# Performance work log

Measured on AMD Instinct MI355X. Metric: run time of the kernel, lower is better.

Reference implementation:

```python
import jax, jax.numpy as jnp
import numpy as np

RADIUS2 = 1.0   # radius=1 -> radius^2
NSAMPLE = 4
EPS = 1e-5


def _ball_group(new_xyz, xyz, feats):
    """Per-batch radius ball query + feature grouping.
    new_xyz: (Nq,3), xyz: (Ns,3), feats: (Ns,C) -> (Nq, NSAMPLE, C)."""
    Ns = xyz.shape[0]
    # squared distances via gemm form to avoid a (Nq,Ns,3) intermediate
    d2 = (jnp.sum(new_xyz**2, -1)[:, None] + jnp.sum(xyz**2, -1)[None, :]
          - 2.0 * new_xyz @ xyz.T)                      # (Nq, Ns)
    within = d2 < RADIUS2
    # first NSAMPLE in-radius indices, in point order (pcdet semantics)
    scores = jnp.where(within, -jnp.arange(Ns, dtype=jnp.int32), -Ns)
    vals, _ = jax.lax.top_k(scores, NSAMPLE)
    idx = -vals                                         # (Nq, NSAMPLE); Ns == invalid slot
    valid = idx < Ns
    empty = ~valid[:, 0]                                # no neighbor at all
    idx = jnp.where(valid, idx, idx[:, :1])             # pad with first found neighbor
    idx = jnp.where(empty[:, None], 0, idx)
    grouped = feats[idx]                                # (Nq, NSAMPLE, C) irregular gather
    return jnp.where(empty[:, None, None], 0.0, grouped)


def _bn(x, g, b, axes):
    # BatchNorm1d training-mode stats (biased var); channel axis = 1
    m = jnp.mean(x, axes, keepdims=True)
    v = jnp.var(x, axes, keepdims=True)
    shape = [1] * x.ndim
    shape[1] = -1
    return g.reshape(shape) * (x - m) * jax.lax.rsqrt(v + EPS) + b.reshape(shape)


def _forward(x, conv1_w, conv1_b, bn_g, bn_b, fc1_w, fc1_b, fc_ce_w, fc_ce_b,
             fc2_w, fc2_b, fc_lwh_w, fc_lwh_b, fc3_w, fc3_b, fc_theta_w, fc_theta_b):
    B, T, N, C = x.shape
    new_xyz = x[:, 0, :, :3]                              # (B, N, 3) query points
    xyz = x[:, 1:, :, :3].reshape(B, (T - 1) * N, 3)      # (B, Ns, 3) source points
    feats = x[:, 1:].reshape(B, (T - 1) * N, C)           # (B, Ns, C) source features
    grouped = jax.vmap(_ball_group)(new_xyz, xyz, feats)  # (B, N, NSAMPLE, C)
    g = grouped.reshape(B * N, NSAMPLE, C).transpose(0, 2, 1)  # (M, C, NSAMPLE)
    # shared conv1d (kernel=1) + BN + max-pool over the group
    h = jnp.einsum('mcs,oc->mos', g, conv1_w) + conv1_b[None, :, None]
    h = _bn(h, bn_g, bn_b, (0, 2))
    h = jnp.max(h, axis=-1)                               # (M, D)
    feature = h.reshape(B, N, -1)
    # three FC heads, all reusing bn1 (as in the original module)
    x1 = jax.nn.relu(_bn(h @ fc1_w.T + fc1_b, bn_g, bn_b, (0,)))
    x_ce = x1 @ fc_ce_w.T + fc_ce_b
    x2 = jax.nn.relu(_bn(h @ fc2_w.T + fc2_b, bn_g, bn_b, (0,)))
    x_lwh = x2 @ fc_lwh_w.T + fc_lwh_b
    x3 = jax.nn.relu(_bn(h @ fc3_w.T + fc3_b, bn_g, bn_b, (0,)))
    x_th = x3 @ fc_theta_w.T + fc_theta_b
    out = jnp.concatenate([x_ce, x_lwh, x_th], -1).reshape(B, N, 7)
    return out, feature


def setup_inputs() -> dict:
    key = jax.random.key(0)
    ks = jax.random.split(key, 16)
    B, T, N, C, D = 2, 5, 4096, 16, 128
    x = jax.random.normal(ks[0], (B, T, N, C), jnp.float32)
    w = lambda k, s: jax.random.normal(k, s, jnp.float32) * 0.05
    return dict(
        x=x,
        conv1_w=w(ks[1], (D, C)), conv1_b=w(ks[2], (D,)),
        bn_g=jnp.ones((D,), jnp.float32), bn_b=jnp.zeros((D,), jnp.float32),
        fc1_w=w(ks[3], (D, D)), fc1_b=w(ks[4], (D,)),
        fc_ce_w=w(ks[5], (3, D)), fc_ce_b=w(ks[6], (3,)),
        fc2_w=w(ks[7], (D, D)), fc2_b=w(ks[8], (D,)),
        fc_lwh_w=w(ks[9], (3, D)), fc_lwh_b=w(ks[10], (3,)),
        fc3_w=w(ks[11], (D, D)), fc3_b=w(ks[12], (D,)),
        fc_theta_w=w(ks[13], (1, D)), fc_theta_b=w(ks[14], (1,)),
    )


def reference(x, conv1_w, conv1_b, bn_g, bn_b, fc1_w, fc1_b, fc_ce_w, fc_ce_b,
              fc2_w, fc2_b, fc_lwh_w, fc_lwh_b, fc3_w, fc3_b, fc_theta_w, fc_theta_b):
    return _forward(x, conv1_w, conv1_b, bn_g, bn_b, fc1_w, fc1_b, fc_ce_w, fc_ce_b,
                    fc2_w, fc2_b, fc_lwh_w, fc_lwh_b, fc3_w, fc3_b, fc_theta_w, fc_theta_b)
```

## Files before the change

### kernel.cpp

```cpp
#include <hip/hip_runtime.h>

#define B_   2
#define T_   5
#define N_   4096
#define C_   16
#define D_   128
#define S_   4
#define NS_  16384
#define M_   8192
#define EPS_ 1e-5f
#define NPART 32

#define HX_OFF   0u
#define HN_OFF   1048576u
#define Y_OFF    2097152u
#define ST_OFF   5242880u
#define WL_OFF   5275648u
#define ID4_OFF  5283848u
#define WP_OFF   5316616u
#define PK_OFF   5365768u

#define OUT_FEAT 57344

__global__ __launch_bounds__(256) void k_prep(const float* __restrict__ x,
                                              const float* __restrict__ fw1,
                                              const float* __restrict__ fw2,
                                              const float* __restrict__ fw3,
                                              float* __restrict__ st,
                                              int* __restrict__ wcnt,
                                              float4* __restrict__ wp,
                                              float4* __restrict__ pk4) {
    int tid = threadIdx.x;
    if (blockIdx.x < 128) {
        int row = blockIdx.x * 256 + tid;
        int b = row >> 14, j = row & 16383;
        const float* p = x + (size_t)b * (T_ * N_ * C_) + N_ * C_ + (size_t)j * 16;
        float4 v = *(const float4*)p;
        float pn = (v.x * v.x + v.y * v.y) + v.z * v.z;
        pk4[row] = make_float4(v.x, v.y, v.z, pn);
        return;
    }
    int pb = blockIdx.x - 128;
    int t0 = pb * 256 + tid;
    #pragma unroll
    for (int i = 0; i < 8; i++) st[t0 + 4096 * i] = 0.0f;
    if (pb == 0 && tid == 0) wcnt[0] = 0;
    int o = t0 >> 5, c4 = t0 & 31;
    const float* fws[3] = { fw1, fw2, fw3 };
    #pragma unroll
    for (int k = 0; k < 3; k++)
        wp[k * 4096 + c4 * 128 + o] = *(const float4*)(fws[k] + o * 128 + c4 * 4);
}

__global__ __launch_bounds__(256) void k_ball1(const float* __restrict__ x,
                                               const float* __restrict__ w,
                                               const float* __restrict__ bias,
                                               const float4* __restrict__ pk4,
                                               float* __restrict__ hx,
                                               float* __restrict__ hn,
                                               float* __restrict__ st,
                                               int* __restrict__ wcnt,
                                               int* __restrict__ wl,
                                               int4* __restrict__ id4) {
    int tid = threadIdx.x;
    int wid = tid >> 6, lane = tid & 63;
    __shared__ float red[2][512];

    float wc0[16], wc1[16];
    #pragma unroll
    for (int j = 0; j < 4; j++) {
        float4 a = *(const float4*)(w + lane * 16 + j * 4);
        float4 b2 = *(const float4*)(w + (lane + 64) * 16 + j * 4);
        wc0[j*4+0] = a.x;  wc0[j*4+1] = a.y;  wc0[j*4+2] = a.z;  wc0[j*4+3] = a.w;
        wc1[j*4+0] = b2.x; wc1[j*4+1] = b2.y; wc1[j*4+2] = b2.z; wc1[j*4+3] = b2.w;
    }
    float bo0 = bias[lane], bo1 = bias[lane + 64];

    float asum0 = 0.0f, asq0 = 0.0f, asum1 = 0.0f, asq1 = 0.0f;
    for (int qi = 0; qi < 4; qi++) {
        int m = (blockIdx.x * 4 + wid) * 4 + qi;
        int b = m >> 12, q = m & (N_ - 1);
        const float* xb = x + (size_t)b * (T_ * N_ * C_);
        const float* pts = xb + N_ * C_;
        const float4* pk = pk4 + b * 16384;
        float qx = xb[q * 16 + 0];
        float qy = xb[q * 16 + 1];
        float qz = xb[q * 16 + 2];
        float qn = (qx * qx + qy * qy) + qz * qz;

        float4 pv[8];
        #pragma unroll
        for (int u = 0; u < 8; u++) pv[u] = pk[u * 64 + lane];
        unsigned long long mk[8];
        #pragma unroll
        for (int u = 0; u < 8; u++) {
            float dot = (qx * pv[u].x + qy * pv[u].y) + qz * pv[u].z;
            mk[u] = __ballot((qn + pv[u].w) - 2.0f * dot < 1.0f);
        }

        int i0 = 0, i1 = 0, i2 = 0, i3 = 0, cnt = 0;
        unsigned long long m0 = mk[0];
        if (__builtin_popcountll(m0) >= 4) {
            i0 = __builtin_ctzll(m0); m0 &= m0 - 1;
            i1 = __builtin_ctzll(m0); m0 &= m0 - 1;
            i2 = __builtin_ctzll(m0); m0 &= m0 - 1;
            i3 = __builtin_ctzll(m0);
            cnt = 4;
        } else {
            #pragma unroll
            for (int u = 0; u < 8; u++) {
                unsigned long long mask = mk[u];
                while (mask && cnt < 4) {
                    int id = u * 64 + __builtin_ctzll(mask);
                    if (cnt == 0)      i0 = id;
                    else if (cnt == 1) i1 = id;
                    else if (cnt == 2) i2 = id;
                    else               i3 = id;
                    cnt++;
                    mask &= (mask - 1);
                }
            }
        }

        if (cnt >= 4) {
            int ids[4] = {i0, i1, i2, i3};
            float a0[4], a1[4];
            #pragma unroll
            for (int s = 0; s < 4; s++) {
                const float* rp = pts + (size_t)ids[s] * 16;
                float4 r0 = *(const float4*)(rp);
                float4 r1 = *(const float4*)(rp + 4);
                float4 r2 = *(const float4*)(rp + 8);
                float4 r3 = *(const float4*)(rp + 12);
                float s0 = bo0, s1 = bo1;
                s0 += wc0[0] * r0.x;  s0 += wc0[1] * r0.y;  s0 += wc0[2] * r0.z;  s0 += wc0[3] * r0.w;
                s0 += wc0[4] * r1.x;  s0 += wc0[5] * r1.y;  s0 += wc0[6] * r1.z;  s0 += wc0[7] * r1.w;
                s0 += wc0[8] * r2.x;  s0 += wc0[9] * r2.y;  s0 += wc0[10] * r2.z; s0 += wc0[11] * r2.w;
                s0 += wc0[12] * r3.x; s0 += wc0[13] * r3.y; s0 += wc0[14] * r3.z; s0 += wc0[15] * r3.w;
                s1 += wc1[0] * r0.x;  s1 += wc1[1] * r0.y;  s1 += wc1[2] * r0.z;  s1 += wc1[3] * r0.w;
                s1 += wc1[4] * r1.x;  s1 += wc1[5] * r1.y;  s1 += wc1[6] * r1.z;  s1 += wc1[7] * r1.w;
                s1 += wc1[8] * r2.x;  s1 += wc1[9] * r2.y;  s1 += wc1[10] * r2.z; s1 += wc1[11] * r2.w;
                s1 += wc1[12] * r3.x; s1 += wc1[13] * r3.y; s1 += wc1[14] * r3.z; s1 += wc1[15] * r3.w;
                a0[s] = s0; a1[s] = s1;
            }
            hx[(size_t)m * 128 + lane]      = fmaxf(fmaxf(a0[0], a0[1]), fmaxf(a0[2], a0[3]));
            hx[(size_t)m * 128 + 64 + lane] = fmaxf(fmaxf(a1[0], a1[1]), fmaxf(a1[2], a1[3]));
            hn[(size_t)m * 128 + lane]      = fminf(fminf(a0[0], a0[1]), fminf(a0[2], a0[3]));
            hn[(size_t)m * 128 + 64 + lane] = fminf(fminf(a1[0], a1[1]), fminf(a1[2], a1[3]));
            asum0 += (a0[0] + a0[1]) + (a0[2] + a0[3]);
            asq0  += (a0[0] * a0[0] + a0[1] * a0[1]) + (a0[2] * a0[2] + a0[3] * a0[3]);
            asum1 += (a1[0] + a1[1]) + (a1[2] + a1[3]);
            asq1  += (a1[0] * a1[0] + a1[1] * a1[1]) + (a1[2] * a1[2] + a1[3] * a1[3]);
        } else {
            if (lane == 0) {
                int idx = atomicAdd(wcnt, 1);
                wl[idx] = m;
                id4[m] = make_int4(i0, i1, i2, cnt);
            }
        }
    }

    red[0][wid * 128 + lane]      = asum0;
    red[0][wid * 128 + 64 + lane] = asum1;
    red[1][wid * 128 + lane]      = asq0;
    red[1][wid * 128 + 64 + lane] = asq1;
    __syncthreads();
    if (tid < 128) {
        float* stp = st + (blockIdx.x & (NPART - 1)) * 256;
        float s0 = (red[0][tid] + red[0][128 + tid]) + (red[0][256 + tid] + red[0][384 + tid]);
        float s1 = (red[1][tid] + red[1][128 + tid]) + (red[1][256 + tid] + red[1][384 + tid]);
        atomicAdd(&stp[tid], s0);
        atomicAdd(&stp[128 + tid], s1);
    }
}

__global__ __launch_bounds__(256) void k_ball2(const float* __restrict__ x,
                                               const float* __restrict__ w,
                                               const float* __restrict__ bias,
                                               const float4* __restrict__ pk4,
                                               float* __restrict__ hx,
                                               float* __restrict__ hn,
                                               float* __restrict__ st,
                                               const int* __restrict__ wcnt,
                                               const int* __restrict__ wl,
                                               const int4* __restrict__ id4) {
    int tid = threadIdx.x;
    int wid = tid >> 6, lane = tid & 63;
    __shared__ int sCnt[4];
    __shared__ int sIds[4][4];

    float wc0[16], wc1[16];
    float bo0 = 0.0f, bo1 = 0.0f;
    if (wid == 0) {
        #pragma unroll
        for (int j = 0; j < 4; j++) {
            float4 a = *(const float4*)(w + lane * 16 + j * 4);
            float4 b2 = *(const float4*)(w + (lane + 64) * 16 + j * 4);
            wc0[j*4+0] = a.x;  wc0[j*4+1] = a.y;  wc0[j*4+2] = a.z;  wc0[j*4+3] = a.w;
            wc1[j*4+0] = b2.x; wc1[j*4+1] = b2.y; wc1[j*4+2] = b2.z; wc1[j*4+3] = b2.w;
        }
        bo0 = bias[lane]; bo1 = bias[lane + 64];
    }
    float asum0 = 0.0f, asq0 = 0.0f, asum1 = 0.0f, asq1 = 0.0f;

    int nstrag = *wcnt;
    for (int e = blockIdx.x; e < nstrag; e += gridDim.x) {
        int m = wl[e];
        int b = m >> 12, q = m & (N_ - 1);
        const float* xb = x + (size_t)b * (T_ * N_ * C_);
        const float* pts = xb + N_ * C_;
        const float4* pk = pk4 + b * 16384;
        float qx = xb[q * 16 + 0];
        float qy = xb[q * 16 + 1];
        float qz = xb[q * 16 + 2];
        float qn = (qx * qx + qy * qy) + qz * qz;

        int cstart = 1 + 8 * wid;
        int cend = cstart + 8; if (cend > 32) cend = 32;
        int y0 = 0, y1 = 0, y2 = 0, y3 = 0;
        int myc = 0;
        for (int c = cstart; c < cend && myc < 4; c += 2) {
            bool two = (c + 1 < cend);
            float4 pva[8], pvb[8];
            #pragma unroll
            for (int u = 0; u < 8; u++) pva[u] = pk[c * 512 + u * 64 + lane];
            if (two) {
                #pragma unroll
                for (int u = 0; u < 8; u++) pvb[u] = pk[(c + 1) * 512 + u * 64 + lane];
            }
            unsigned long long ma[8], mb[8];
            #pragma unroll
            for (int u = 0; u < 8; u++) {
                float dot = (qx * pva[u].x + qy * pva[u].y) + qz * pva[u].z;
                ma[u] = __ballot((qn + pva[u].w) - 2.0f * dot < 1.0f);
            }
            if (two) {
                #pragma unroll
                for (int u = 0; u < 8; u++) {
                    float dot = (qx * pvb[u].x + qy * pvb[u].y) + qz * pvb[u].z;
                    mb[u] = __ballot((qn + pvb[u].w) - 2.0f * dot < 1.0f);
                }
            }
            #pragma unroll
            for (int u = 0; u < 8; u++) {
                unsigned long long mask = ma[u];
                while (mask && myc < 4) {
                    int id = c * 512 + u * 64 + __builtin_ctzll(mask);
                    if (myc == 0)      y0 = id;
                    else if (myc == 1) y1 = id;
                    else if (myc == 2) y2 = id;
                    else               y3 = id;
                    myc++;
                    mask &= (mask - 1);
                }
            }
            if (two) {
                #pragma unroll
                for (int u = 0; u < 8; u++) {
                    unsigned long long mask = mb[u];
                    while (mask && myc < 4) {
                        int id = (c + 1) * 512 + u * 64 + __builtin_ctzll(mask);
                        if (myc == 0)      y0 = id;
                        else if (myc == 1) y1 = id;
                        else if (myc == 2) y2 = id;
                        else               y3 = id;
                        myc++;
                        mask &= (mask - 1);
                    }
                }
            }
        }
        if (lane == 0) {
            sCnt[wid] = myc;
            sIds[wid][0] = y0; sIds[wid][1] = y1;
            sIds[wid][2] = y2; sIds[wid][3] = y3;
        }
        __syncthreads();

        if (wid == 0) {
            int4 p1 = id4[m];
            int f0 = 0, f1 = 0, f2 = 0, f3 = 0;
            int fc = p1.w;
            if (fc > 0) f0 = p1.x;
            if (fc > 1) f1 = p1.y;
            if (fc > 2) f2 = p1.z;
            #pragma unroll
            for (int w2 = 0; w2 < 4; w2++) {
                int c2 = sCnt[w2];
                #pragma unroll
                for (int i = 0; i < 4; i++) {
                    if (i < c2 && fc < 4) {
                        int id = sIds[w2][i];
                        if (fc == 0)      f0 = id;
                        else if (fc == 1) f1 = id;
                        else if (fc == 2) f2 = id;
                        else              f3 = id;
                        fc++;
                    }
                }
            }
            if (fc >= 1) {
                if (fc <= 1) f1 = f0;
                if (fc <= 2) f2 = f0;
                if (fc <= 3) f3 = f0;
            }
            int fin[4] = {f0, f1, f2, f3};
            float a0[4], a1[4];
            if (fc == 0) {
                #pragma unroll
                for (int s = 0; s < 4; s++) { a0[s] = bo0; a1[s] = bo1; }
            } else {
                #pragma unroll
                for (int s = 0; s < 4; s++) {
                    const float* rp = pts + (size_t)fin[s] * 16;
                    float4 r0 = *(const float4*)(rp);
                    float4 r1 = *(const float4*)(rp + 4);
                    float4 r2 = *(const float4*)(rp + 8);
                    float4 r3 = *(const float4*)(rp + 12);
                    float s0 = bo0, s1 = bo1;
                    s0 += wc0[0] * r0.x;  s0 += wc0[1] * r0.y;  s0 += wc0[2] * r0.z;  s0 += wc0[3] * r0.w;
                    s0 += wc0[4] * r1.x;  s0 += wc0[5] * r1.y;  s0 += wc0[6] * r1.z;  s0 += wc0[7] * r1.w;
                    s0 += wc0[8] * r2.x;  s0 += wc0[9] * r2.y;  s0 += wc0[10] * r2.z; s0 += wc0[11] * r2.w;
                    s0 += wc0[12] * r3.x; s0 += wc0[13] * r3.y; s0 += wc0[14] * r3.z; s0 += wc0[15] * r3.w;
                    s1 += wc1[0] * r0.x;  s1 += wc1[1] * r0.y;  s1 += wc1[2] * r0.z;  s1 += wc1[3] * r0.w;
                    s1 += wc1[4] * r1.x;  s1 += wc1[5] * r1.y;  s1 += wc1[6] * r1.z;  s1 += wc1[7] * r1.w;
                    s1 += wc1[8] * r2.x;  s1 += wc1[9] * r2.y;  s1 += wc1[10] * r2.z; s1 += wc1[11] * r2.w;
                    s1 += wc1[12] * r3.x; s1 += wc1[13] * r3.y; s1 += wc1[14] * r3.z; s1 += wc1[15] * r3.w;
                    a0[s] = s0; a1[s] = s1;
                }
            }
            hx[(size_t)m * 128 + lane]      = fmaxf(fmaxf(a0[0], a0[1]), fmaxf(a0[2], a0[3]));
            hx[(size_t)m * 128 + 64 + lane] = fmaxf(fmaxf(a1[0], a1[1]), fmaxf(a1[2], a1[3]));
            hn[(size_t)m * 128 + lane]      = fminf(fminf(a0[0], a0[1]), fminf(a0[2], a0[3]));
            hn[(size_t)m * 128 + 64 + lane] = fminf(fminf(a1[0], a1[1]), fminf(a1[2], a1[3]));
            asum0 += (a0[0] + a0[1]) + (a0[2] + a0[3]);
            asq0  += (a0[0] * a0[0] + a0[1] * a0[1]) + (a0[2] * a0[2] + a0[3] * a0[3]);
            asum1 += (a1[0] + a1[1]) + (a1[2] + a1[3]);
            asq1  += (a1[0] * a1[0] + a1[1] * a1[1]) + (a1[2] * a1[2] + a1[3] * a1[3]);
        }
        __syncthreads();
    }
    if (wid == 0 && (int)blockIdx.x < nstrag) {
        float* stp = st + (blockIdx.x & (NPART - 1)) * 256;
        atomicAdd(&stp[lane], asum0);
        atomicAdd(&stp[64 + lane], asum1);
        atomicAdd(&stp[128 + lane], asq0);
        atomicAdd(&stp[192 + lane], asq1);
    }
}

__global__ __launch_bounds__(256) void k_fc(const float* __restrict__ hx,
                                            const float* __restrict__ hn,
                                            float* __restrict__ st,
                                            const float4* __restrict__ wp,
                                            const float* __restrict__ b1,
                                            const float* __restrict__ b2,
                                            const float* __restrict__ b3,
                                            const float* __restrict__ bng,
                                            const float* __restrict__ bnb,
                                            float* __restrict__ y,
                                            float* __restrict__ out) {
    int tid = threadIdx.x;
    int m0 = blockIdx.x * 16;
    __shared__ float hs[2048];
    __shared__ float scsh[256];

    if (tid < 128) {
        float s = 0.0f, q2 = 0.0f;
        #pragma unroll
        for (int p = 0; p < NPART; p++) {
            s  += st[p * 256 + tid];
            q2 += st[p * 256 + 128 + tid];
        }
        float mean = s * (1.0f / 32768.0f);
        float var = q2 * (1.0f / 32768.0f) - mean * mean;
        float sc = bng[tid] / sqrtf(fmaxf(var, 0.0f) + EPS_);
        scsh[tid] = sc;
        scsh[128 + tid] = bnb[tid] - mean * sc;
    }
    __syncthreads();

    for (int i = tid; i < 16 * 128; i += 256) {
        int ml = i >> 7, o = i & 127;
        float vx = hx[(size_t)(m0 + ml) * 128 + o];
        float vn = hn[(size_t)(m0 + ml) * 128 + o];
        float sc = scsh[o];
        float r = fmaxf(sc * vx, sc * vn) + scsh[128 + o];
        hs[ml * 128 + o] = r;
        out[(size_t)OUT_FEAT + (size_t)(m0 + ml) * 128 + o] = r;
    }
    __syncthreads();

    int o = tid & 127, gr = tid >> 7;
    int mbase = gr * 8;
    float acc[3][8];
    {
        float bb0 = b1[o], bb1 = b2[o], bb2 = b3[o];
        #pragma unroll
        for (int mm = 0; mm < 8; mm++) {
            acc[0][mm] = bb0; acc[1][mm] = bb1; acc[2][mm] = bb2;
        }
    }
    for (int c4 = 0; c4 < 32; c4++) {
        float4 w1v = wp[c4 * 128 + o];
        float4 w2v = wp[4096 + c4 * 128 + o];
        float4 w3v = wp[8192 + c4 * 128 + o];
        const float* hp = &hs[mbase * 128 + c4 * 4];
        #pragma unroll
        for (int mm = 0; mm < 8; mm++) {
            float4 hv = *(const float4*)(hp + mm * 128);
            acc[0][mm] += w1v.x * hv.x; acc[0][mm] += w1v.y * hv.y;
            acc[0][mm] += w1v.z * hv.z; acc[0][mm] += w1v.w * hv.w;
            acc[1][mm] += w2v.x * hv.x; acc[1][mm] += w2v.y * hv.y;
            acc[1][mm] += w2v.z * hv.z; acc[1][mm] += w2v.w * hv.w;
            acc[2][mm] += w3v.x * hv.x; acc[2][mm] += w3v.y * hv.y;
            acc[2][mm] += w3v.z * hv.z; acc[2][mm] += w3v.w * hv.w;
        }
    }
    __syncthreads();
    float psum[3], psq[3];
    #pragma unroll
    for (int k = 0; k < 3; k++) {
        float s = 0.0f, sq = 0.0f;
        float* yk = y + (size_t)k * M_ * 128;
        #pragma unroll
        for (int mm = 0; mm < 8; mm++) {
            float v = acc[k][mm];
            yk[(size_t)(m0 + mbase + mm) * 128 + o] = v;
            s += v; sq += v * v;
        }
        psum[k] = s; psq[k] = sq;
    }
    #pragma unroll
    for (int k = 0; k < 3; k++) {
        hs[(k * 2 + gr) * 128 + o] = psum[k];
        hs[768 + (k * 2 + gr) * 128 + o] = psq[k];
    }
    __syncthreads();
    float* bp = st + 8192 + (blockIdx.x & (NPART - 1)) * 768;
    for (int t = tid; t < 384; t += 256) {
        int k = t >> 7, oo = t & 127;
        float s  = hs[(k * 2) * 128 + oo] + hs[(k * 2 + 1) * 128 + oo];
        float sq = hs[768 + (k * 2) * 128 + oo] + hs[768 + (k * 2 + 1) * 128 + oo];
        atomicAdd(&bp[k * 256 + oo], s);
        atomicAdd(&bp[k * 256 + 128 + oo], sq);
    }
}

__global__ __launch_bounds__(256) void k_heads(const float* __restrict__ y,
                                               const float* __restrict__ st,
                                               const float* __restrict__ wce, const float* __restrict__ bce,
                                               const float* __restrict__ wlwh, const float* __restrict__ blwh,
                                               const float* __restrict__ wth, const float* __restrict__ bth,
                                               const float* __restrict__ bng, const float* __restrict__ bnb,
                                               float* __restrict__ out) {
    int tid = threadIdx.x;
    __shared__ float bsc[768];
    for (int t = tid; t < 384; t += 256) {
        int k = t >> 7, o = t & 127;
        float s = 0.0f, q2 = 0.0f;
        #pragma unroll
        for (int p = 0; p < NPART; p++) {
            const float* bp = st + 8192 + p * 768 + k * 256;
            s  += bp[o];
            q2 += bp[128 + o];
        }
        float mean = s * (1.0f / 8192.0f);
        float var = q2 * (1.0f / 8192.0f) - mean * mean;
        float sc = bng[o] / sqrtf(fmaxf(var, 0.0f) + EPS_);
        bsc[k * 256 + o] = sc;
        bsc[k * 256 + 128 + o] = bnb[o] - mean * sc;
    }
    __syncthreads();

    int wave = tid >> 6, lane = tid & 63;
    const float* y1 = y;
    const float* y2 = y + (size_t)M_ * D_;
    const float* y3 = y + 2 * (size_t)M_ * D_;
    #pragma unroll
    for (int i = 0; i < 4; i++) {
        int m = blockIdx.x * 16 + wave * 4 + i;
        float p[7] = {0, 0, 0, 0, 0, 0, 0};
        #pragma unroll
        for (int cc = 0; cc < 2; cc++) {
            int c = lane + 64 * cc;
            float v1 = fmaxf(y1[(size_t)m * D_ + c] * bsc[c] + bsc[128 + c], 0.0f);
            float v2 = fmaxf(y2[(size_t)m * D_ + c] * bsc[256 + c] + bsc[384 + c], 0.0f);
            float v3 = fmaxf(y3[(size_t)m * D_ + c] * bsc[512 + c] + bsc[640 + c], 0.0f);
            p[0] += v1 * wce[c];
            p[1] += v1 * wce[128 + c];
            p[2] += v1 * wce[256 + c];
            p[3] += v2 * wlwh[c];
            p[4] += v2 * wlwh[128 + c];
            p[5] += v2 * wlwh[256 + c];
            p[6] += v3 * wth[c];
        }
        #pragma unroll
        for (int off = 32; off > 0; off >>= 1) {
            #pragma unroll
            for (int j = 0; j < 7; j++) p[j] += __shfl_xor(p[j], off);
        }
        if (lane == 0) {
            out[m * 7 + 0] = p[0] + bce[0];
            out[m * 7 + 1] = p[1] + bce[1];
            out[m * 7 + 2] = p[2] + bce[2];
            out[m * 7 + 3] = p[3] + blwh[0];
            out[m * 7 + 4] = p[4] + blwh[1];
            out[m * 7 + 5] = p[5] + blwh[2];
            out[m * 7 + 6] = p[6] + bth[0];
        }
    }
}

extern "C" void kernel_launch(void* const* d_in, const int* in_sizes, int n_in,
                              void* d_out, int out_size, void* d_ws, size_t ws_size,
                              hipStream_t stream) {
    (void)in_sizes; (void)n_in; (void)out_size; (void)ws_size;
    const float* x        = (const float*)d_in[0];
    const float* conv1_w  = (const float*)d_in[1];
    const float* conv1_b  = (const float*)d_in[2];
    const float* bn_g     = (const float*)d_in[3];
    const float* bn_b     = (const float*)d_in[4];
    const float* fc1_w    = (const float*)d_in[5];
    const float* fc1_b    = (const float*)d_in[6];
    const float* fc_ce_w  = (const float*)d_in[7];
    const float* fc_ce_b  = (const float*)d_in[8];
    const float* fc2_w    = (const float*)d_in[9];
    const float* fc2_b    = (const float*)d_in[10];
    const float* fc_lwh_w = (const float*)d_in[11];
    const float* fc_lwh_b = (const float*)d_in[12];
    const float* fc3_w    = (const float*)d_in[13];
    const float* fc3_b    = (const float*)d_in[14];
    const float* fc_th_w  = (const float*)d_in[15];
    const float* fc_th_b  = (const float*)d_in[16];

    float* ws = (float*)d_ws;
    float* hx = ws + HX_OFF;
    float* hn = ws + HN_OFF;
    float* y  = ws + Y_OFF;
    float* st = ws + ST_OFF;
    int*  wcnt = (int*)(ws + WL_OFF);
    int*  wl   = wcnt + 1;
    int4* id4  = (int4*)(ws + ID4_OFF);
    float4* wp  = (float4*)(ws + WP_OFF);
    float4* pk4 = (float4*)(ws + PK_OFF);
    float* out = (float*)d_out;

    hipLaunchKernelGGL(k_prep,  dim3(144),  dim3(256), 0, stream,
                       x, fc1_w, fc2_w, fc3_w, st, wcnt, wp, pk4);
    hipLaunchKernelGGL(k_ball1, dim3(512),  dim3(256), 0, stream,
                       x, conv1_w, conv1_b, pk4, hx, hn, st, wcnt, wl, id4);
    hipLaunchKernelGGL(k_ball2, dim3(512),  dim3(256), 0, stream,
                       x, conv1_w, conv1_b, pk4, hx, hn, st, wcnt, wl, id4);
    hipLaunchKernelGGL(k_fc,    dim3(512),  dim3(256), 0, stream, hx, hn, st, wp,
                       fc1_b, fc2_b, fc3_b, bn_g, bn_b, y, out);
    hipLaunchKernelGGL(k_heads, dim3(512),  dim3(256), 0, stream, y, st,
                       fc_ce_w, fc_ce_b, fc_lwh_w, fc_lwh_b, fc_th_w, fc_th_b, bn_g, bn_b, out);
}
```

Before: 146.9 us.

## Fuse all five stages into one cooperative kernel with grid syncs

Folds prep, ball-query passes, FC and heads into a single cooperative kernel of 512 blocks, with grid-wide barriers between phases in place of separate kernel launches. The intent is to remove per-launch overhead and the gaps between dependent kernels. The fused kernel needs all 512 blocks resident at once and is capped at two blocks per SM by its launch bounds, which can raise register pressure; if the cooperative launch fails, the separate kernels run instead. The prep phase was rewritten to fit a 512-block grid using a global thread index.

```diff
diff --git a/kernel.cpp b/kernel.cpp
--- a/kernel.cpp
+++ b/kernel.cpp
@@ -1,4 +1,7 @@
 #include <hip/hip_runtime.h>
+#include <hip/hip_cooperative_groups.h>
+
+namespace cg = cooperative_groups;
 
 #define B_   2
 #define T_   5
@@ -22,49 +25,44 @@
 
 #define OUT_FEAT 57344
 
-__global__ __launch_bounds__(256) void k_prep(const float* __restrict__ x,
-                                              const float* __restrict__ fw1,
-                                              const float* __restrict__ fw2,
-                                              const float* __restrict__ fw3,
-                                              float* __restrict__ st,
-                                              int* __restrict__ wcnt,
-                                              float4* __restrict__ wp,
-                                              float4* __restrict__ pk4) {
-    int tid = threadIdx.x;
-    if (blockIdx.x < 128) {
-        int row = blockIdx.x * 256 + tid;
-        int b = row >> 14, j = row & 16383;
+
+__device__ __forceinline__ void prep_phase(int bid, int tid,
+    const float* __restrict__ x,
+    const float* __restrict__ fw1, const float* __restrict__ fw2,
+    const float* __restrict__ fw3,
+    float* __restrict__ st, int* __restrict__ wcnt,
+    float4* __restrict__ wp, float4* __restrict__ pk4)
+{
+    int gtid = bid * 256 + tid;
+    if (gtid < 32768) {
+        int b = gtid >> 14, j = gtid & 16383;
         const float* p = x + (size_t)b * (T_ * N_ * C_) + N_ * C_ + (size_t)j * 16;
         float4 v = *(const float4*)p;
         float pn = (v.x * v.x + v.y * v.y) + v.z * v.z;
-        pk4[row] = make_float4(v.x, v.y, v.z, pn);
-        return;
-    }
-    int pb = blockIdx.x - 128;
-    int t0 = pb * 256 + tid;
-    #pragma unroll
-    for (int i = 0; i < 8; i++) st[t0 + 4096 * i] = 0.0f;
-    if (pb == 0 && tid == 0) wcnt[0] = 0;
-    int o = t0 >> 5, c4 = t0 & 31;
-    const float* fws[3] = { fw1, fw2, fw3 };
-    #pragma unroll
-    for (int k = 0; k < 3; k++)
-        wp[k * 4096 + c4 * 128 + o] = *(const float4*)(fws[k] + o * 128 + c4 * 4);
-}
-
-__global__ __launch_bounds__(256) void k_ball1(const float* __restrict__ x,
-                                               const float* __restrict__ w,
-                                               const float* __restrict__ bias,
-                                               const float4* __restrict__ pk4,
-                                               float* __restrict__ hx,
-                                               float* __restrict__ hn,
-                                               float* __restrict__ st,
-                                               int* __restrict__ wcnt,
-                                               int* __restrict__ wl,
-                                               int4* __restrict__ id4) {
-    int tid = threadIdx.x;
+        pk4[gtid] = make_float4(v.x, v.y, v.z, pn);
+    }
+    if (gtid < 4096) {
+        #pragma unroll
+        for (int i = 0; i < 8; i++) st[gtid + 4096 * i] = 0.0f;
+    }
+    if (gtid == 0) wcnt[0] = 0;
+    if (gtid < 12288) {
+        int k = gtid >> 12, t0 = gtid & 4095;
+        int o = t0 >> 5, c4 = t0 & 31;
+        const float* fw = (k == 0) ? fw1 : ((k == 1) ? fw2 : fw3);
+        wp[k * 4096 + c4 * 128 + o] = *(const float4*)(fw + o * 128 + c4 * 4);
+    }
+}
+
+__device__ __forceinline__ void ball1_phase(int bid, int tid, float* smem,
+    const float* __restrict__ x, const float* __restrict__ w,
+    const float* __restrict__ bias, const float4* __restrict__ pk4,
+    float* __restrict__ hx, float* __restrict__ hn, float* __restrict__ st,
+    int* __restrict__ wcnt, int* __restrict__ wl, int4* __restrict__ id4)
+{
     int wid = tid >> 6, lane = tid & 63;
-    __shared__ float red[2][512];
+    float* red0 = smem;
+    float* red1 = smem + 512;
 
     float wc0[16], wc1[16];
     #pragma unroll
@@ -78,7 +76,7 @@
 
     float asum0 = 0.0f, asq0 = 0.0f, asum1 = 0.0f, asq1 = 0.0f;
     for (int qi = 0; qi < 4; qi++) {
-        int m = (blockIdx.x * 4 + wid) * 4 + qi;
+        int m = (bid * 4 + wid) * 4 + qi;
         int b = m >> 12, q = m & (N_ - 1);
         const float* xb = x + (size_t)b * (T_ * N_ * C_);
         const float* pts = xb + N_ * C_;
@@ -160,34 +158,30 @@
         }
     }
 
-    red[0][wid * 128 + lane]      = asum0;
-    red[0][wid * 128 + 64 + lane] = asum1;
-    red[1][wid * 128 + lane]      = asq0;
-    red[1][wid * 128 + 64 + lane] = asq1;
+    red0[wid * 128 + lane]      = asum0;
+    red0[wid * 128 + 64 + lane] = asum1;
+    red1[wid * 128 + lane]      = asq0;
+    red1[wid * 128 + 64 + lane] = asq1;
     __syncthreads();
     if (tid < 128) {
-        float* stp = st + (blockIdx.x & (NPART - 1)) * 256;
-        float s0 = (red[0][tid] + red[0][128 + tid]) + (red[0][256 + tid] + red[0][384 + tid]);
-        float s1 = (red[1][tid] + red[1][128 + tid]) + (red[1][256 + tid] + red[1][384 + tid]);
+        float* stp = st + (bid & (NPART - 1)) * 256;
+        float s0 = (red0[tid] + red0[128 + tid]) + (red0[256 + tid] + red0[384 + tid]);
+        float s1 = (red1[tid] + red1[128 + tid]) + (red1[256 + tid] + red1[384 + tid]);
         atomicAdd(&stp[tid], s0);
         atomicAdd(&stp[128 + tid], s1);
     }
 }
 
-__global__ __launch_bounds__(256) void k_ball2(const float* __restrict__ x,
-                                               const float* __restrict__ w,
-                                               const float* __restrict__ bias,
-                                               const float4* __restrict__ pk4,
-                                               float* __restrict__ hx,
-                                               float* __restrict__ hn,
-                                               float* __restrict__ st,
-                                               const int* __restrict__ wcnt,
-                                               const int* __restrict__ wl,
-                                               const int4* __restrict__ id4) {
-    int tid = threadIdx.x;
+__device__ __forceinline__ void ball2_phase(int bid, int tid, float* smem,
+    const float* __restrict__ x, const float* __restrict__ w,
+    const float* __restrict__ bias, const float4* __restrict__ pk4,
+    float* __restrict__ hx, float* __restrict__ hn, float* __restrict__ st,
+    const int* __restrict__ wcnt, const int* __restrict__ wl,
+    const int4* __restrict__ id4)
+{
     int wid = tid >> 6, lane = tid & 63;
-    __shared__ int sCnt[4];
-    __shared__ int sIds[4][4];
+    int* sCnt = (int*)smem;
+    int* sIds = (int*)smem + 4;
 
     float wc0[16], wc1[16];
     float bo0 = 0.0f, bo1 = 0.0f;
@@ -204,7 +198,7 @@
     float asum0 = 0.0f, asq0 = 0.0f, asum1 = 0.0f, asq1 = 0.0f;
 
     int nstrag = *wcnt;
-    for (int e = blockIdx.x; e < nstrag; e += gridDim.x) {
+    for (int e = bid; e < nstrag; e += 512) {
         int m = wl[e];
         int b = m >> 12, q = m & (N_ - 1);
         const float* xb = x + (size_t)b * (T_ * N_ * C_);
@@ -272,8 +266,8 @@
         }
         if (lane == 0) {
             sCnt[wid] = myc;
-            sIds[wid][0] = y0; sIds[wid][1] = y1;
-            sIds[wid][2] = y2; sIds[wid][3] = y3;
+            sIds[wid * 4 + 0] = y0; sIds[wid * 4 + 1] = y1;
+            sIds[wid * 4 + 2] = y2; sIds[wid * 4 + 3] = y3;
         }
         __syncthreads();
 
@@ -290,7 +284,7 @@
                 #pragma unroll
                 for (int i = 0; i < 4; i++) {
                     if (i < c2 && fc < 4) {
-                        int id = sIds[w2][i];
+                        int id = sIds[w2 * 4 + i];
                         if (fc == 0)      f0 = id;
                         else if (fc == 1) f1 = id;
                         else if (fc == 2) f2 = id;
@@ -340,8 +334,8 @@
         }
         __syncthreads();
     }
-    if (wid == 0 && (int)blockIdx.x < nstrag) {
-        float* stp = st + (blockIdx.x & (NPART - 1)) * 256;
+    if (wid == 0 && bid < nstrag) {
+        float* stp = st + (bid & (NPART - 1)) * 256;
         atomicAdd(&stp[lane], asum0);
         atomicAdd(&stp[64 + lane], asum1);
         atomicAdd(&stp[128 + lane], asq0);
@@ -349,21 +343,17 @@
     }
 }
 
-__global__ __launch_bounds__(256) void k_fc(const float* __restrict__ hx,
-                                            const float* __restrict__ hn,
-                                            float* __restrict__ st,
-                                            const float4* __restrict__ wp,
-                                            const float* __restrict__ b1,
-                                            const float* __restrict__ b2,
-                                            const float* __restrict__ b3,
-                                            const float* __restrict__ bng,
-                                            const float* __restrict__ bnb,
-                                            float* __restrict__ y,
-                                            float* __restrict__ out) {
-    int tid = threadIdx.x;
-    int m0 = blockIdx.x * 16;
-    __shared__ float hs[2048];
-    __shared__ float scsh[256];
+__device__ __forceinline__ void fc_phase(int bid, int tid, float* smem,
+    const float* __restrict__ hx, const float* __restrict__ hn,
+    float* __restrict__ st, const float4* __restrict__ wp,
+    const float* __restrict__ b1, const float* __restrict__ b2,
+    const float* __restrict__ b3, const float* __restrict__ bng,
+    const float* __restrict__ bnb, float* __restrict__ y,
+    float* __restrict__ out)
+{
+    int m0 = bid * 16;
+    float* hs = smem;
+    float* scsh = smem + 2048;
 
     if (tid < 128) {
         float s = 0.0f, q2 = 0.0f;
@@ -437,7 +427,7 @@
         hs[768 + (k * 2 + gr) * 128 + o] = psq[k];
     }
     __syncthreads();
-    float* bp = st + 8192 + (blockIdx.x & (NPART - 1)) * 768;
+    float* bp = st + 8192 + (bid & (NPART - 1)) * 768;
     for (int t = tid; t < 384; t += 256) {
         int k = t >> 7, oo = t & 127;
         float s  = hs[(k * 2) * 128 + oo] + hs[(k * 2 + 1) * 128 + oo];
@@ -447,15 +437,15 @@
     }
 }
 
-__global__ __launch_bounds__(256) void k_heads(const float* __restrict__ y,
-                                               const float* __restrict__ st,
-                                               const float* __restrict__ wce, const float* __restrict__ bce,
-                                               const float* __restrict__ wlwh, const float* __restrict__ blwh,
-                                               const float* __restrict__ wth, const float* __restrict__ bth,
-                                               const float* __restrict__ bng, const float* __restrict__ bnb,
-                                               float* __restrict__ out) {
-    int tid = threadIdx.x;
-    __shared__ float bsc[768];
+__device__ __forceinline__ void heads_phase(int bid, int tid, float* smem,
+    const float* __restrict__ y, const float* __restrict__ st,
+    const float* __restrict__ wce, const float* __restrict__ bce,
+    const float* __restrict__ wlwh, const float* __restrict__ blwh,
+    const float* __restrict__ wth, const float* __restrict__ bth,
+    const float* __restrict__ bng, const float* __restrict__ bnb,
+    float* __restrict__ out)
+{
+    float* bsc = smem;
     for (int t = tid; t < 384; t += 256) {
         int k = t >> 7, o = t & 127;
         float s = 0.0f, q2 = 0.0f;
@@ -479,7 +469,7 @@
     const float* y3 = y + 2 * (size_t)M_ * D_;
     #pragma unroll
     for (int i = 0; i < 4; i++) {
-        int m = blockIdx.x * 16 + wave * 4 + i;
+        int m = bid * 16 + wave * 4 + i;
         float p[7] = {0, 0, 0, 0, 0, 0, 0};
         #pragma unroll
         for (int cc = 0; cc < 2; cc++) {
@@ -510,6 +500,73 @@
             out[m * 7 + 6] = p[6] + bth[0];
         }
     }
+}
+
+__global__ __launch_bounds__(256, 2) void k_fused(
+    const float* x, const float* conv1_w, const float* conv1_b,
+    const float* fw1, const float* fw2, const float* fw3,
+    const float* b1, const float* b2, const float* b3,
+    const float* bng, const float* bnb,
+    const float* wce, const float* bce,
+    const float* wlwh, const float* blwh,
+    const float* wth, const float* bth,
+    float* hx, float* hn, float* y, float* st,
+    int* wcnt, int* wl, int4* id4, float4* wp, float4* pk4,
+    float* out)
+{
+    __shared__ float smem[2304];
+    int bid = blockIdx.x, tid = threadIdx.x;
+    cg::grid_group grid = cg::this_grid();
+
+    prep_phase(bid, tid, x, fw1, fw2, fw3, st, wcnt, wp, pk4);
+    grid.sync();
+    ball1_phase(bid, tid, smem, x, conv1_w, conv1_b, pk4, hx, hn, st, wcnt, wl, id4);
+    grid.sync();
+    ball2_phase(bid, tid, smem, x, conv1_w, conv1_b, pk4, hx, hn, st, wcnt, wl, id4);
+    grid.sync();
+    fc_phase(bid, tid, smem, hx, hn, st, wp, b1, b2, b3, bng, bnb, y, out);
+    grid.sync();
+    heads_phase(bid, tid, smem, y, st, wce, bce, wlwh, blwh, wth, bth, bng, bnb, out);
+}
+
+__global__ __launch_bounds__(256) void k_prep(const float* __restrict__ x,
+    const float* __restrict__ fw1, const float* __restrict__ fw2,
+    const float* __restrict__ fw3, float* __restrict__ st,
+    int* __restrict__ wcnt, float4* __restrict__ wp, float4* __restrict__ pk4) {
+    prep_phase(blockIdx.x, threadIdx.x, x, fw1, fw2, fw3, st, wcnt, wp, pk4);
+}
+__global__ __launch_bounds__(256) void k_ball1(const float* __restrict__ x,
+    const float* __restrict__ w, const float* __restrict__ bias,
+    const float4* __restrict__ pk4, float* __restrict__ hx, float* __restrict__ hn,
+    float* __restrict__ st, int* __restrict__ wcnt, int* __restrict__ wl,
+    int4* __restrict__ id4) {
+    __shared__ float smem[1024];
+    ball1_phase(blockIdx.x, threadIdx.x, smem, x, w, bias, pk4, hx, hn, st, wcnt, wl, id4);
+}
+__global__ __launch_bounds__(256) void k_ball2(const float* __restrict__ x,
+    const float* __restrict__ w, const float* __restrict__ bias,
+    const float4* __restrict__ pk4, float* __restrict__ hx, float* __restrict__ hn,
+    float* __restrict__ st, const int* __restrict__ wcnt, const int* __restrict__ wl,
+    const int4* __restrict__ id4) {
+    __shared__ float smem[32];
+    ball2_phase(blockIdx.x, threadIdx.x, smem, x, w, bias, pk4, hx, hn, st, wcnt, wl, id4);
+}
+__global__ __launch_bounds__(256) void k_fc(const float* __restrict__ hx,
+    const float* __restrict__ hn, float* __restrict__ st, const float4* __restrict__ wp,
+    const float* __restrict__ b1, const float* __restrict__ b2,
+    const float* __restrict__ b3, const float* __restrict__ bng,
+    const float* __restrict__ bnb, float* __restrict__ y, float* __restrict__ out) {
+    __shared__ float smem[2304];
+    fc_phase(blockIdx.x, threadIdx.x, smem, hx, hn, st, wp, b1, b2, b3, bng, bnb, y, out);
+}
+__global__ __launch_bounds__(256) void k_heads(const float* __restrict__ y,
+    const float* __restrict__ st, const float* __restrict__ wce,
+    const float* __restrict__ bce, const float* __restrict__ wlwh,
+    const float* __restrict__ blwh, const float* __restrict__ wth,
+    const float* __restrict__ bth, const float* __restrict__ bng,
+    const float* __restrict__ bnb, float* __restrict__ out) {
+    __shared__ float smem[768];
+    heads_phase(blockIdx.x, threadIdx.x, smem, y, st, wce, bce, wlwh, blwh, wth, bth, bng, bnb, out);
 }
 
 extern "C" void kernel_launch(void* const* d_in, const int* in_sizes, int n_in,
@@ -546,14 +603,33 @@
     float4* pk4 = (float4*)(ws + PK_OFF);
     float* out = (float*)d_out;
 
-    hipLaunchKernelGGL(k_prep,  dim3(144),  dim3(256), 0, stream,
-                       x, fc1_w, fc2_w, fc3_w, st, wcnt, wp, pk4);
-    hipLaunchKernelGGL(k_ball1, dim3(512),  dim3(256), 0, stream,
-                       x, conv1_w, conv1_b, pk4, hx, hn, st, wcnt, wl, id4);
-    hipLaunchKernelGGL(k_ball2, dim3(512),  dim3(256), 0, stream,
-                       x, conv1_w, conv1_b, pk4, hx, hn, st, wcnt, wl, id4);
-    hipLaunchKernelGGL(k_fc,    dim3(512),  dim3(256), 0, stream, hx, hn, st, wp,
-                       fc1_b, fc2_b, fc3_b, bn_g, bn_b, y, out);
-    hipLaunchKernelGGL(k_heads, dim3(512),  dim3(256), 0, stream, y, st,
-                       fc_ce_w, fc_ce_b, fc_lwh_w, fc_lwh_b, fc_th_w, fc_th_b, bn_g, bn_b, out);
-}
+    void* args[] = {
+        (void*)&x, (void*)&conv1_w, (void*)&conv1_b,
+        (void*)&fc1_w, (void*)&fc2_w, (void*)&fc3_w,
+        (void*)&fc1_b, (void*)&fc2_b, (void*)&fc3_b,
+        (void*)&bn_g, (void*)&bn_b,
+        (void*)&fc_ce_w, (void*)&fc_ce_b,
+        (void*)&fc_lwh_w, (void*)&fc_lwh_b,
+        (void*)&fc_th_w, (void*)&fc_th_b,
+        (void*)&hx, (void*)&hn, (void*)&y, (void*)&st,
+        (void*)&wcnt, (void*)&wl, (void*)&id4, (void*)&wp, (void*)&pk4,
+        (void*)&out
+    };
+    hipError_t err = hipLaunchCooperativeKernel((const void*)k_fused,
+                                                dim3(512), dim3(256),
+                                                args, 0, stream);
+    if (err != hipSuccess) {
+        (void)hipGetLastError();
+        hipLaunchKernelGGL(k_prep,  dim3(512), dim3(256), 0, stream,
+                           x, fc1_w, fc2_w, fc3_w, st, wcnt, wp, pk4);
+        hipLaunchKernelGGL(k_ball1, dim3(512), dim3(256), 0, stream,
+                           x, conv1_w, conv1_b, pk4, hx, hn, st, wcnt, wl, id4);
+        hipLaunchKernelGGL(k_ball2, dim3(512), dim3(256), 0, stream,
+                           x, conv1_w, conv1_b, pk4, hx, hn, st, wcnt, wl, id4);
+        hipLaunchKernelGGL(k_fc,    dim3(512), dim3(256), 0, stream, hx, hn, st, wp,
+                           fc1_b, fc2_b, fc3_b, bn_g, bn_b, y, out);
+        hipLaunchKernelGGL(k_heads, dim3(512), dim3(256), 0, stream, y, st,
+                           fc_ce_w, fc_ce_b, fc_lwh_w, fc_lwh_b, fc_th_w, fc_th_b,
+                           bn_g, bn_b, out);
+    }
+}
```

New measurement: 394.4 us. 2.69x slower.

## Fuse prep kernel into ball-query kernel and zero stats via memset

Applied to the files above, without the earlier changes.

Removes the separate prep kernel. Its point packing and FC weight transposition are spread across the threads of the first ball-query kernel, and the stats and counter are zeroed with an async memset. The first ball kernel now builds point norms straight from the input and doubles its grid, with two queries per warp instead of four. This is meant to cut a launch and a serial dependency. The cost is some redundant per-warp point loads and norm computation.

```diff
diff --git a/kernel.cpp b/kernel.cpp
--- a/kernel.cpp
+++ b/kernel.cpp
@@ -22,40 +22,14 @@
 
 #define OUT_FEAT 57344
 
-__global__ __launch_bounds__(256) void k_prep(const float* __restrict__ x,
-                                              const float* __restrict__ fw1,
-                                              const float* __restrict__ fw2,
-                                              const float* __restrict__ fw3,
-                                              float* __restrict__ st,
-                                              int* __restrict__ wcnt,
-                                              float4* __restrict__ wp,
-                                              float4* __restrict__ pk4) {
-    int tid = threadIdx.x;
-    if (blockIdx.x < 128) {
-        int row = blockIdx.x * 256 + tid;
-        int b = row >> 14, j = row & 16383;
-        const float* p = x + (size_t)b * (T_ * N_ * C_) + N_ * C_ + (size_t)j * 16;
-        float4 v = *(const float4*)p;
-        float pn = (v.x * v.x + v.y * v.y) + v.z * v.z;
-        pk4[row] = make_float4(v.x, v.y, v.z, pn);
-        return;
-    }
-    int pb = blockIdx.x - 128;
-    int t0 = pb * 256 + tid;
-    #pragma unroll
-    for (int i = 0; i < 8; i++) st[t0 + 4096 * i] = 0.0f;
-    if (pb == 0 && tid == 0) wcnt[0] = 0;
-    int o = t0 >> 5, c4 = t0 & 31;
-    const float* fws[3] = { fw1, fw2, fw3 };
-    #pragma unroll
-    for (int k = 0; k < 3; k++)
-        wp[k * 4096 + c4 * 128 + o] = *(const float4*)(fws[k] + o * 128 + c4 * 4);
-}
-
 __global__ __launch_bounds__(256) void k_ball1(const float* __restrict__ x,
                                                const float* __restrict__ w,
                                                const float* __restrict__ bias,
-                                               const float4* __restrict__ pk4,
+                                               const float* __restrict__ fw1,
+                                               const float* __restrict__ fw2,
+                                               const float* __restrict__ fw3,
+                                               float4* __restrict__ wp,
+                                               float4* __restrict__ pk4,
                                                float* __restrict__ hx,
                                                float* __restrict__ hn,
                                                float* __restrict__ st,
@@ -63,8 +37,24 @@
                                                int* __restrict__ wl,
                                                int4* __restrict__ id4) {
     int tid = threadIdx.x;
+    int bid = blockIdx.x;
     int wid = tid >> 6, lane = tid & 63;
     __shared__ float red[2][512];
+
+    if (tid < 32) {
+        int row = bid * 32 + tid;
+        int b = row >> 14, j = row & 16383;
+        const float* p = x + (size_t)b * (T_ * N_ * C_) + N_ * C_ + (size_t)j * 16;
+        float4 v = *(const float4*)p;
+        float pn = (v.x * v.x + v.y * v.y) + v.z * v.z;
+        pk4[row] = make_float4(v.x, v.y, v.z, pn);
+    } else if (tid < 44) {
+        int i = bid * 12 + (tid - 32);
+        int k = i >> 12, t0 = i & 4095;
+        int o = t0 >> 5, c4 = t0 & 31;
+        const float* fw = (k == 0) ? fw1 : ((k == 1) ? fw2 : fw3);
+        wp[k * 4096 + c4 * 128 + o] = *(const float4*)(fw + o * 128 + c4 * 4);
+    }
 
     float wc0[16], wc1[16];
     #pragma unroll
@@ -76,21 +66,29 @@
     }
     float bo0 = bias[lane], bo1 = bias[lane + 64];
 
+    int mbase = (bid * 4 + wid) * 2;
+    int b = mbase >> 12;
+    const float* xb = x + (size_t)b * (T_ * N_ * C_);
+    const float* pts = xb + N_ * C_;
+    float4 pv[8];
+    #pragma unroll
+    for (int u = 0; u < 8; u++) {
+        const float* p = pts + (size_t)(u * 64 + lane) * 16;
+        float4 v = *(const float4*)p;
+        float pn = (v.x * v.x + v.y * v.y) + v.z * v.z;
+        pv[u] = make_float4(v.x, v.y, v.z, pn);
+    }
+
     float asum0 = 0.0f, asq0 = 0.0f, asum1 = 0.0f, asq1 = 0.0f;
-    for (int qi = 0; qi < 4; qi++) {
-        int m = (blockIdx.x * 4 + wid) * 4 + qi;
-        int b = m >> 12, q = m & (N_ - 1);
-        const float* xb = x + (size_t)b * (T_ * N_ * C_);
-        const float* pts = xb + N_ * C_;
-        const float4* pk = pk4 + b * 16384;
+    #pragma unroll
+    for (int qi = 0; qi < 2; qi++) {
+        int m = mbase + qi;
+        int q = m & (N_ - 1);
         float qx = xb[q * 16 + 0];
         float qy = xb[q * 16 + 1];
         float qz = xb[q * 16 + 2];
         float qn = (qx * qx + qy * qy) + qz * qz;
 
-        float4 pv[8];
-        #pragma unroll
-        for (int u = 0; u < 8; u++) pv[u] = pk[u * 64 + lane];
         unsigned long long mk[8];
         #pragma unroll
         for (int u = 0; u < 8; u++) {
@@ -166,7 +164,7 @@
     red[1][wid * 128 + 64 + lane] = asq1;
     __syncthreads();
     if (tid < 128) {
-        float* stp = st + (blockIdx.x & (NPART - 1)) * 256;
+        float* stp = st + (bid & (NPART - 1)) * 256;
         float s0 = (red[0][tid] + red[0][128 + tid]) + (red[0][256 + tid] + red[0][384 + tid]);
         float s1 = (red[1][tid] + red[1][128 + tid]) + (red[1][256 + tid] + red[1][384 + tid]);
         atomicAdd(&stp[tid], s0);
@@ -546,10 +544,11 @@
     float4* pk4 = (float4*)(ws + PK_OFF);
     float* out = (float*)d_out;
 
-    hipLaunchKernelGGL(k_prep,  dim3(144),  dim3(256), 0, stream,
-                       x, fc1_w, fc2_w, fc3_w, st, wcnt, wp, pk4);
-    hipLaunchKernelGGL(k_ball1, dim3(512),  dim3(256), 0, stream,
-                       x, conv1_w, conv1_b, pk4, hx, hn, st, wcnt, wl, id4);
+    hipMemsetAsync(st, 0, (32768 + 1) * sizeof(float), stream);
+
+    hipLaunchKernelGGL(k_ball1, dim3(1024), dim3(256), 0, stream,
+                       x, conv1_w, conv1_b, fc1_w, fc2_w, fc3_w, wp, pk4,
+                       hx, hn, st, wcnt, wl, id4);
     hipLaunchKernelGGL(k_ball2, dim3(512),  dim3(256), 0, stream,
                        x, conv1_w, conv1_b, pk4, hx, hn, st, wcnt, wl, id4);
     hipLaunchKernelGGL(k_fc,    dim3(512),  dim3(256), 0, stream, hx, hn, st, wp,
```

Measured after the change: 152.2 us. +3.6%, slower.
